# Kernel optimization log

Measured on AMD Instinct MI355X. Metric: run time of the kernel, lower is better.

The kernel has to match this reference:

```python
import jax, jax.numpy as jnp
import numpy as np

B, C, CI, H, W = 8, 256, 128, 48, 48


def conv1x1(x, w, b):
    # x: (B,C,H,W), w: (CI,C), b: (CI,)
    return jnp.einsum('bchw,oc->bohw', x, w) + b[None, :, None, None]


def setup_inputs() -> dict:
    key = jax.random.key(0)
    ks = jax.random.split(key, 14)
    s = 1.0 / np.sqrt(C)
    d = {
        'x_1': jax.random.normal(ks[0], (B, C, H, W), jnp.float32),
        'x_2': jax.random.normal(ks[1], (B, C, H, W), jnp.float32),
    }
    names = ['v1', 'k1', 'q1', 'v2', 'k2', 'q2']
    for i, n in enumerate(names):
        d['w_' + n] = jax.random.uniform(ks[2 + 2 * i], (CI, C), jnp.float32, -s, s)
        d['b_' + n] = jax.random.uniform(ks[3 + 2 * i], (CI,), jnp.float32, -s, s)
    return d


def reference(x_1, x_2, w_v1, b_v1, w_k1, b_k1, w_q1, b_q1,
              w_v2, b_v2, w_k2, b_k2, w_q2, b_q2):
    b, ci, h, w = x_1.shape[0], w_v1.shape[0], x_1.shape[2], x_1.shape[3]
    n = h * w
    V1 = conv1x1(x_1, w_v1, b_v1).reshape(b, ci, n)
    K1 = conv1x1(x_1, w_k1, b_k1).reshape(b, ci, n)
    Q1 = conv1x1(x_1, w_q1, b_q1).reshape(b, ci, n)
    V2 = conv1x1(x_2, w_v2, b_v2).reshape(b, ci, n)
    K2 = conv1x1(x_2, w_k2, b_k2).reshape(b, ci, n)
    Q2 = conv1x1(x_2, w_q2, b_q2).reshape(b, ci, n)
    # sigmoid-gated cross attention, (B, N, N)
    R12 = jax.nn.sigmoid(jnp.einsum('bcn,bcm->bnm', Q1, K2))
    R21 = jax.nn.sigmoid(jnp.einsum('bcn,bcm->bnm', Q2, K1))
    Fu1 = jnp.einsum('bnm,bcm->bcn', R12, V2).reshape(b, ci, h, w)
    Fu2 = jnp.einsum('bnm,bcm->bcn', R21, V1).reshape(b, ci, h, w)
    y_1 = jnp.concatenate([x_1, Fu1], axis=1)
    y_2 = jnp.concatenate([x_2, Fu2], axis=1)
    return (y_1, y_2)
```

## Files before the change

### kernel.cpp

```cpp
#include <hip/hip_runtime.h>
#include <hip/hip_bf16.h>


typedef __bf16 bf16;
typedef __bf16 bf16x8 __attribute__((ext_vector_type(8)));
typedef __bf16 bf16x4 __attribute__((ext_vector_type(4)));
typedef float f32x4 __attribute__((ext_vector_type(4)));
typedef float f32x16 __attribute__((ext_vector_type(16)));
typedef unsigned int u32x4 __attribute__((ext_vector_type(4)));

#define NB 8
#define NC 256
#define NCI 128
#define NHW 2304
#define NT32 72

__global__ __launch_bounds__(256) void wconv_kernel(
    const float* __restrict__ w0, const float* __restrict__ w1,
    const float* __restrict__ w2, const float* __restrict__ w3,
    const float* __restrict__ w4, const float* __restrict__ w5,
    bf16* __restrict__ dst)
{
    int idx = (blockIdx.x * 256 + threadIdx.x) * 8;
    int m = idx >> 15;
    int off = idx & 32767;
    const float* w = (m == 0) ? w0 : (m == 1) ? w1 : (m == 2) ? w2
                   : (m == 3) ? w3 : (m == 4) ? w4 : w5;
    f32x4 a0 = *(const f32x4*)(w + off);
    f32x4 a1 = *(const f32x4*)(w + off + 4);
    bf16x8 o;
    #pragma unroll
    for (int j = 0; j < 4; ++j) { o[j] = (bf16)a0[j]; o[4 + j] = (bf16)a1[j]; }
    *(bf16x8*)(dst + idx) = o;
}

__global__ __launch_bounds__(256) void qkv_kernel(
    const float* __restrict__ x1, const float* __restrict__ x2,
    const bf16* __restrict__ wb,
    const float* __restrict__ bv1, const float* __restrict__ bk1, const float* __restrict__ bq1,
    const float* __restrict__ bv2, const float* __restrict__ bk2, const float* __restrict__ bq2,
    bf16* __restrict__ Qt, bf16* __restrict__ Kt, bf16* __restrict__ Vt,
    float* __restrict__ out)
{
    __shared__ __align__(16) bf16 Xt[32 * 264];

    int gid = blockIdx.x;
    int nt = gid % NT32;
    int s = (gid / NT32) & 1;
    int b = gid / (2 * NT32);
    int n0 = nt * 32;

    const float* x = s ? x2 : x1;
    const bf16* wv = wb + (size_t)(s * 3 + 0) * (NCI * NC);
    const bf16* wk = wb + (size_t)(s * 3 + 1) * (NCI * NC);
    const bf16* wq = wb + (size_t)(s * 3 + 2) * (NCI * NC);
    const float* bv = s ? bv2 : bv1;
    const float* bk = s ? bk2 : bk1;
    const float* bq = s ? bq2 : bq1;
    float* outy = out + (size_t)s * (NB * 384 * NHW);

    int tid = threadIdx.x;
    {
        int n_off = (tid & 3) * 8;
        int c0l = tid >> 2;
        #pragma unroll
        for (int i = 0; i < 4; ++i) {
            int c = c0l + i * 64;
            const float* src = x + ((size_t)(b * NC + c) * NHW + n0 + n_off);
            f32x4 a0 = *(const f32x4*)src;
            f32x4 a1 = *(const f32x4*)(src + 4);
            float* dsty = outy + ((size_t)(b * 384 + c) * NHW + n0 + n_off);
            *(f32x4*)dsty = a0;
            *(f32x4*)(dsty + 4) = a1;
            #pragma unroll
            for (int j = 0; j < 4; ++j) {
                Xt[(n_off + j) * 264 + c] = (bf16)a0[j];
                Xt[(n_off + 4 + j) * 264 + c] = (bf16)a1[j];
            }
        }
    }
    __syncthreads();

    int lane = tid & 63;
    int wid = tid >> 6;
    int row = lane & 15, quad = lane >> 4;
    int ci_base = wid * 32;

    f32x4 acc[3][2][2];
    #pragma unroll
    for (int t = 0; t < 3; ++t)
        #pragma unroll
        for (int mi = 0; mi < 2; ++mi)
            #pragma unroll
            for (int j = 0; j < 2; ++j)
                acc[t][mi][j] = (f32x4){0.f, 0.f, 0.f, 0.f};

    const bf16* wptr[3] = {wq, wk, wv};
    #pragma unroll
    for (int ks = 0; ks < 8; ++ks) {
        int c0 = ks * 32 + quad * 8;
        bf16x8 bfrag[2];
        #pragma unroll
        for (int j = 0; j < 2; ++j)
            bfrag[j] = *(const bf16x8*)&Xt[(j * 16 + row) * 264 + c0];
        #pragma unroll
        for (int t = 0; t < 3; ++t) {
            #pragma unroll
            for (int mi = 0; mi < 2; ++mi) {
                bf16x8 afrag = *(const bf16x8*)&wptr[t][(size_t)(ci_base + mi * 16 + row) * NC + c0];
                #pragma unroll
                for (int j = 0; j < 2; ++j)
                    acc[t][mi][j] = __builtin_amdgcn_mfma_f32_16x16x32_bf16(
                        afrag, bfrag[j], acc[t][mi][j], 0, 0, 0);
            }
        }
    }

    size_t qkbase = ((size_t)s * NB + b) * NHW * NCI;
    size_t vbase  = ((size_t)s * NB + b) * NCI * NHW;
    #pragma unroll
    for (int mi = 0; mi < 2; ++mi) {
        int ci0 = ci_base + mi * 16 + quad * 4;
        f32x4 bq4 = *(const f32x4*)&bq[ci0];
        f32x4 bk4 = *(const f32x4*)&bk[ci0];
        f32x4 bv4 = *(const f32x4*)&bv[ci0];
        #pragma unroll
        for (int j = 0; j < 2; ++j) {
            int n = n0 + j * 16 + row;
            bf16x4 pk;
            #pragma unroll
            for (int r = 0; r < 4; ++r) pk[r] = (bf16)(acc[0][mi][j][r] + bq4[r]);
            *(bf16x4*)&Qt[qkbase + (size_t)n * NCI + ci0] = pk;
            #pragma unroll
            for (int r = 0; r < 4; ++r) pk[r] = (bf16)(acc[1][mi][j][r] + bk4[r]);
            *(bf16x4*)&Kt[qkbase + (size_t)n * NCI + ci0] = pk;
            #pragma unroll
            for (int r = 0; r < 4; ++r)
                Vt[vbase + (size_t)(ci0 + r) * NHW + n] = (bf16)(acc[2][mi][j][r] + bv4[r]);
        }
    }
}

__global__ __launch_bounds__(512, 2) void attn_kernel(
    const bf16* __restrict__ Qt, const bf16* __restrict__ Kt, const bf16* __restrict__ Vt,
    float* __restrict__ out)
{
    __shared__ __align__(16) bf16 SMEM[40960];
    bf16* KQ = SMEM;
    bf16* VQ = SMEM + 16384;
    bf16* QL = SMEM + 32768;

    int gid = blockIdx.x;
    int pair = (gid & 7) * 2 + ((gid >> 3) & 1);
    int nb = gid >> 4;
    int dir = pair & 1;
    int b = pair >> 1;

    int tid = threadIdx.x;
    int lane = tid & 63;
    int w = tid >> 6;
    int ns = w & 1;
    int mq = w >> 1;
    int col = lane & 31;
    int hi = lane >> 5;

    int sq = dir, skv = dir ^ 1;
    const bf16* q = Qt + ((size_t)sq  * NB + b) * (NHW * NCI);
    const bf16* k = Kt + ((size_t)skv * NB + b) * (NHW * NCI);
    const bf16* v = Vt + ((size_t)skv * NB + b) * (NCI * NHW);
    float* outy = out + (size_t)dir * (NB * 384 * NHW) + ((size_t)b * 384 + 256) * NHW;

    #pragma unroll
    for (int i = 0; i < 2; ++i) {
        int c = tid + i * 512;
        int qr = c >> 4, qc = c & 15;
        bf16x8 t = *(const bf16x8*)&q[(size_t)(nb * 64 + qr) * NCI + qc * 8];
        *(bf16x8*)&QL[qr * 128 + ((qc ^ (qr & 15)) * 8)] = t;
    }

    int kgoff[4], vgoff[4], kloff[4], vloff[4];
    #pragma unroll
    for (int i = 0; i < 4; ++i) {
        int c = tid + i * 512;
        int qd = c >> 9, cc = c & 511;
        int kr = cc >> 4, kc = cc & 15;
        kgoff[i] = (qd * 576 + kr) * NCI + kc * 8;
        kloff[i] = qd * 4096 + kr * 128 + ((kc ^ (kr & 15)) * 8);
        int vr = cc >> 2, vc = cc & 3;
        vgoff[i] = vr * NHW + qd * 576 + vc * 8;
        vloff[i] = qd * 4096 + vr * 32 + ((vc ^ ((vr >> 1) & 3)) * 8);
    }

    int nw = nb * 64 + ns * 32;

    f32x16 o0, o1, o2, o3;
    #pragma unroll
    for (int j = 0; j < 16; ++j) { o0[j] = 0.f; o1[j] = 0.f; o2[j] = 0.f; o3[j] = 0.f; }

    bf16x8 rk[4], rv[4];
    #pragma unroll
    for (int i = 0; i < 4; ++i) {
        rk[i] = *(const bf16x8*)(k + kgoff[i]);
        rv[i] = *(const bf16x8*)(v + vgoff[i]);
    }

    int krd = mq * 4096 + col * 128;
    int qrd = (ns * 32 + col) * 128;
    int cswz = col & 15;
    int vsw = (col >> 1) & 3;
    int vrd = mq * 4096 + col * 32;

    for (int it = 0; it < 18; ++it) {
        __syncthreads();
        #pragma unroll
        for (int i = 0; i < 4; ++i) {
            *(bf16x8*)&KQ[kloff[i]] = rk[i];
            *(bf16x8*)&VQ[vloff[i]] = rv[i];
        }
        __syncthreads();

        f32x16 s;
        #pragma unroll
        for (int j = 0; j < 16; ++j) s[j] = 0.f;

        __builtin_amdgcn_s_setprio(1);
        #pragma unroll
        for (int kq = 0; kq < 8; ++kq) {
            int ch = ((2 * kq + hi) ^ cswz) * 8;
            bf16x8 kf = *(const bf16x8*)&KQ[krd + ch];
            bf16x8 qf = *(const bf16x8*)&QL[qrd + ch];
            s = __builtin_amdgcn_mfma_f32_32x32x16_bf16(kf, qf, s, 0, 0, 0);
        }
        __builtin_amdgcn_s_setprio(0);

        float p[16];
        #pragma unroll
        for (int r = 0; r < 16; ++r) {
            float e = __expf(-s[r]);
            p[r] = __builtin_amdgcn_rcpf(1.0f + e);
        }
        u32x4 pbw[2];
        #pragma unroll
        for (int kst = 0; kst < 2; ++kst) {
            unsigned int a0, a1, b0, b1;
            asm("v_cvt_pk_bf16_f32 %0, %1, %2" : "=v"(a0) : "v"(p[8*kst+0]), "v"(p[8*kst+1]));
            asm("v_cvt_pk_bf16_f32 %0, %1, %2" : "=v"(a1) : "v"(p[8*kst+2]), "v"(p[8*kst+3]));
            asm("v_cvt_pk_bf16_f32 %0, %1, %2" : "=v"(b0) : "v"(p[8*kst+4]), "v"(p[8*kst+5]));
            asm("v_cvt_pk_bf16_f32 %0, %1, %2" : "=v"(b1) : "v"(p[8*kst+6]), "v"(p[8*kst+7]));
            asm volatile("v_permlane32_swap_b32 %0, %1" : "+v"(a0), "+v"(b0));
            asm volatile("v_permlane32_swap_b32 %0, %1" : "+v"(a1), "+v"(b1));
            pbw[kst] = (u32x4){a0, a1, b0, b1};
        }

        if (it < 17) {
            size_t ko = (size_t)(it + 1) * 4096;
            int vo = (it + 1) * 32;
            #pragma unroll
            for (int i = 0; i < 4; ++i) {
                rk[i] = *(const bf16x8*)(k + ko + kgoff[i]);
                rv[i] = *(const bf16x8*)(v + vo + vgoff[i]);
            }
        }

        __builtin_amdgcn_s_setprio(1);
        #pragma unroll
        for (int km = 0; km < 2; ++km) {
            bf16x8 pf = __builtin_bit_cast(bf16x8, pbw[km]);
            int mch = ((2 * km + hi) ^ vsw) * 8;
            {
                bf16x8 vf = *(const bf16x8*)&VQ[vrd + 0 * 1024 + mch];
                o0 = __builtin_amdgcn_mfma_f32_32x32x16_bf16(vf, pf, o0, 0, 0, 0);
            }
            {
                bf16x8 vf = *(const bf16x8*)&VQ[vrd + 1 * 1024 + mch];
                o1 = __builtin_amdgcn_mfma_f32_32x32x16_bf16(vf, pf, o1, 0, 0, 0);
            }
            {
                bf16x8 vf = *(const bf16x8*)&VQ[vrd + 2 * 1024 + mch];
                o2 = __builtin_amdgcn_mfma_f32_32x32x16_bf16(vf, pf, o2, 0, 0, 0);
            }
            {
                bf16x8 vf = *(const bf16x8*)&VQ[vrd + 3 * 1024 + mch];
                o3 = __builtin_amdgcn_mfma_f32_32x32x16_bf16(vf, pf, o3, 0, 0, 0);
            }
        }
        __builtin_amdgcn_s_setprio(0);
    }

    float* RED = (float*)SMEM;

    auto wpart = [&](float* buf, const f32x16& a, int cb) {
        #pragma unroll
        for (int g = 0; g < 4; ++g) {
            f32x4 v4;
            #pragma unroll
            for (int j = 0; j < 4; ++j) v4[j] = a[g * 4 + j];
            *(f32x4*)&buf[lane * 64 + (((cb * 4 + g) ^ (lane & 15)) * 4)] = v4;
        }
    };
    auto rpart = [&](float* buf, f32x16& a, int cb) {
        #pragma unroll
        for (int g = 0; g < 4; ++g) {
            f32x4 v4 = *(const f32x4*)&buf[lane * 64 + (((cb * 4 + g) ^ (lane & 15)) * 4)];
            #pragma unroll
            for (int j = 0; j < 4; ++j) a[g * 4 + j] += v4[j];
        }
    };

    __syncthreads();
    if (mq >= 2) {
        float* buf = RED + (ns * 2 + (mq & 1)) * 4096;
        wpart(buf, o0, 0); wpart(buf, o1, 1); wpart(buf, o2, 2); wpart(buf, o3, 3);
    }
    __syncthreads();
    if (mq < 2) {
        float* buf = RED + (ns * 2 + mq) * 4096;
        rpart(buf, o0, 0); rpart(buf, o1, 1); rpart(buf, o2, 2); rpart(buf, o3, 3);
    }
    __syncthreads();
    if (mq == 1) {
        float* buf = RED + ns * 4096;
        wpart(buf, o0, 0); wpart(buf, o1, 1); wpart(buf, o2, 2); wpart(buf, o3, 3);
    }
    __syncthreads();
    if (mq == 0) {
        float* buf = RED + ns * 4096;
        rpart(buf, o0, 0); rpart(buf, o1, 1); rpart(buf, o2, 2); rpart(buf, o3, 3);
        #pragma unroll
        for (int r = 0; r < 16; ++r) {
            int cr = (r & 3) + 8 * (r >> 2) + 4 * hi;
            outy[(size_t)(0 * 32 + cr) * NHW + nw + col] = o0[r];
            outy[(size_t)(1 * 32 + cr) * NHW + nw + col] = o1[r];
            outy[(size_t)(2 * 32 + cr) * NHW + nw + col] = o2[r];
            outy[(size_t)(3 * 32 + cr) * NHW + nw + col] = o3[r];
        }
    }
}

extern "C" void kernel_launch(void* const* d_in, const int* in_sizes, int n_in,
                              void* d_out, int out_size, void* d_ws, size_t ws_size,
                              hipStream_t stream) {
    const float* x1  = (const float*)d_in[0];
    const float* x2  = (const float*)d_in[1];
    const float* wv1 = (const float*)d_in[2];  const float* bv1 = (const float*)d_in[3];
    const float* wk1 = (const float*)d_in[4];  const float* bk1 = (const float*)d_in[5];
    const float* wq1 = (const float*)d_in[6];  const float* bq1 = (const float*)d_in[7];
    const float* wv2 = (const float*)d_in[8];  const float* bv2 = (const float*)d_in[9];
    const float* wk2 = (const float*)d_in[10]; const float* bk2 = (const float*)d_in[11];
    const float* wq2 = (const float*)d_in[12]; const float* bq2 = (const float*)d_in[13];
    float* out = (float*)d_out;

    size_t per = (size_t)2 * NB * NHW * NCI;
    bf16* Qt = (bf16*)d_ws;
    bf16* Kt = Qt + per;
    bf16* Vt = Kt + per;
    bf16* wb = Vt + per;

    wconv_kernel<<<dim3(96), dim3(256), 0, stream>>>(wv1, wk1, wq1, wv2, wk2, wq2, wb);

    qkv_kernel<<<dim3(NB * 2 * NT32), dim3(256), 0, stream>>>(
        x1, x2, wb, bv1, bk1, bq1, bv2, bk2, bq2, Qt, Kt, Vt, out);

    attn_kernel<<<dim3(NB * 2 * 36), dim3(512), 0, stream>>>(Qt, Kt, Vt, out);
}
```

Before: 244.1 us.

## Restructure attention block to 4 waves with Q fragments held in registers

```diff
diff --git a/kernel.cpp b/kernel.cpp
--- a/kernel.cpp
+++ b/kernel.cpp
@@ -141,18 +141,17 @@
     }
 }
 
-__global__ __launch_bounds__(512, 2) void attn_kernel(
+__global__ __launch_bounds__(256, 3) void attn_kernel(
     const bf16* __restrict__ Qt, const bf16* __restrict__ Kt, const bf16* __restrict__ Vt,
     float* __restrict__ out)
 {
-    __shared__ __align__(16) bf16 SMEM[40960];
-    bf16* KQ = SMEM;
-    bf16* VQ = SMEM + 16384;
-    bf16* QL = SMEM + 32768;
+    __shared__ __align__(16) bf16 SMEM[16384];
+    bf16* KH = SMEM;
+    bf16* VH = SMEM + 8192;
 
     int gid = blockIdx.x;
     int pair = (gid & 7) * 2 + ((gid >> 3) & 1);
-    int nb = gid >> 4;
+    int nt = gid >> 4;
     int dir = pair & 1;
     int b = pair >> 1;
 
@@ -160,7 +159,7 @@
     int lane = tid & 63;
     int w = tid >> 6;
     int ns = w & 1;
-    int mq = w >> 1;
+    int mh = w >> 1;
     int col = lane & 31;
     int hi = lane >> 5;
 
@@ -170,28 +169,25 @@
     const bf16* v = Vt + ((size_t)skv * NB + b) * (NCI * NHW);
     float* outy = out + (size_t)dir * (NB * 384 * NHW) + ((size_t)b * 384 + 256) * NHW;
 
-    #pragma unroll
-    for (int i = 0; i < 2; ++i) {
-        int c = tid + i * 512;
-        int qr = c >> 4, qc = c & 15;
-        bf16x8 t = *(const bf16x8*)&q[(size_t)(nb * 64 + qr) * NCI + qc * 8];
-        *(bf16x8*)&QL[qr * 128 + ((qc ^ (qr & 15)) * 8)] = t;
-    }
-
     int kgoff[4], vgoff[4], kloff[4], vloff[4];
     #pragma unroll
     for (int i = 0; i < 4; ++i) {
-        int c = tid + i * 512;
-        int qd = c >> 9, cc = c & 511;
+        int c = tid + i * 256;
+        int hs = c >> 9;
+        int cc = c & 511;
         int kr = cc >> 4, kc = cc & 15;
-        kgoff[i] = (qd * 576 + kr) * NCI + kc * 8;
-        kloff[i] = qd * 4096 + kr * 128 + ((kc ^ (kr & 15)) * 8);
+        kgoff[i] = (hs * 1152 + kr) * NCI + kc * 8;
+        kloff[i] = hs * 4096 + kr * 128 + ((kc ^ (kr & 15)) * 8);
         int vr = cc >> 2, vc = cc & 3;
-        vgoff[i] = vr * NHW + qd * 576 + vc * 8;
-        vloff[i] = qd * 4096 + vr * 32 + ((vc ^ ((vr >> 1) & 3)) * 8);
-    }
-
-    int nw = nb * 64 + ns * 32;
+        vgoff[i] = vr * NHW + hs * 1152 + vc * 8;
+        vloff[i] = hs * 4096 + vr * 32 + ((vc ^ ((vr >> 1) & 3)) * 8);
+    }
+
+    int nw = nt * 64 + ns * 32;
+    bf16x8 qf[8];
+    #pragma unroll
+    for (int kq = 0; kq < 8; ++kq)
+        qf[kq] = *(const bf16x8*)&q[(size_t)(nw + col) * NCI + kq * 16 + hi * 8];
 
     f32x16 o0, o1, o2, o3;
     #pragma unroll
@@ -204,20 +200,28 @@
         rv[i] = *(const bf16x8*)(v + vgoff[i]);
     }
 
-    int krd = mq * 4096 + col * 128;
-    int qrd = (ns * 32 + col) * 128;
+    const bf16* KB = &KH[mh * 4096];
+    const bf16* VB = &VH[mh * 4096];
     int cswz = col & 15;
     int vsw = (col >> 1) & 3;
-    int vrd = mq * 4096 + col * 32;
-
-    for (int it = 0; it < 18; ++it) {
+
+    for (int it = 0; it < 36; ++it) {
         __syncthreads();
         #pragma unroll
         for (int i = 0; i < 4; ++i) {
-            *(bf16x8*)&KQ[kloff[i]] = rk[i];
-            *(bf16x8*)&VQ[vloff[i]] = rv[i];
+            *(bf16x8*)&KH[kloff[i]] = rk[i];
+            *(bf16x8*)&VH[vloff[i]] = rv[i];
         }
         __syncthreads();
+        if (it < 35) {
+            size_t ko = (size_t)(it + 1) * 32 * NCI;
+            int vo = (it + 1) * 32;
+            #pragma unroll
+            for (int i = 0; i < 4; ++i) {
+                rk[i] = *(const bf16x8*)(k + ko + kgoff[i]);
+                rv[i] = *(const bf16x8*)(v + vo + vgoff[i]);
+            }
+        }
 
         f32x16 s;
         #pragma unroll
@@ -226,10 +230,8 @@
         __builtin_amdgcn_s_setprio(1);
         #pragma unroll
         for (int kq = 0; kq < 8; ++kq) {
-            int ch = ((2 * kq + hi) ^ cswz) * 8;
-            bf16x8 kf = *(const bf16x8*)&KQ[krd + ch];
-            bf16x8 qf = *(const bf16x8*)&QL[qrd + ch];
-            s = __builtin_amdgcn_mfma_f32_32x32x16_bf16(kf, qf, s, 0, 0, 0);
+            bf16x8 kf = *(const bf16x8*)&KB[col * 128 + (((2 * kq + hi) ^ cswz) * 8)];
+            s = __builtin_amdgcn_mfma_f32_32x32x16_bf16(kf, qf[kq], s, 0, 0, 0);
         }
         __builtin_amdgcn_s_setprio(0);
 
@@ -252,35 +254,25 @@
             pbw[kst] = (u32x4){a0, a1, b0, b1};
         }
 
-        if (it < 17) {
-            size_t ko = (size_t)(it + 1) * 4096;
-            int vo = (it + 1) * 32;
-            #pragma unroll
-            for (int i = 0; i < 4; ++i) {
-                rk[i] = *(const bf16x8*)(k + ko + kgoff[i]);
-                rv[i] = *(const bf16x8*)(v + vo + vgoff[i]);
-            }
-        }
-
         __builtin_amdgcn_s_setprio(1);
         #pragma unroll
         for (int km = 0; km < 2; ++km) {
             bf16x8 pf = __builtin_bit_cast(bf16x8, pbw[km]);
             int mch = ((2 * km + hi) ^ vsw) * 8;
             {
-                bf16x8 vf = *(const bf16x8*)&VQ[vrd + 0 * 1024 + mch];
+                bf16x8 vf = *(const bf16x8*)&VB[(0 * 32 + col) * 32 + mch];
                 o0 = __builtin_amdgcn_mfma_f32_32x32x16_bf16(vf, pf, o0, 0, 0, 0);
             }
             {
-                bf16x8 vf = *(const bf16x8*)&VQ[vrd + 1 * 1024 + mch];
+                bf16x8 vf = *(const bf16x8*)&VB[(1 * 32 + col) * 32 + mch];
                 o1 = __builtin_amdgcn_mfma_f32_32x32x16_bf16(vf, pf, o1, 0, 0, 0);
             }
             {
-                bf16x8 vf = *(const bf16x8*)&VQ[vrd + 2 * 1024 + mch];
+                bf16x8 vf = *(const bf16x8*)&VB[(2 * 32 + col) * 32 + mch];
                 o2 = __builtin_amdgcn_mfma_f32_32x32x16_bf16(vf, pf, o2, 0, 0, 0);
             }
             {
-                bf16x8 vf = *(const bf16x8*)&VQ[vrd + 3 * 1024 + mch];
+                bf16x8 vf = *(const bf16x8*)&VB[(3 * 32 + col) * 32 + mch];
                 o3 = __builtin_amdgcn_mfma_f32_32x32x16_bf16(vf, pf, o3, 0, 0, 0);
             }
         }
@@ -288,43 +280,30 @@
     }
 
     float* RED = (float*)SMEM;
-
-    auto wpart = [&](float* buf, const f32x16& a, int cb) {
+    float* buf = RED + ns * 4096;
+
+    auto wpart = [&](float* bp, const f32x16& a, int cb) {
         #pragma unroll
         for (int g = 0; g < 4; ++g) {
             f32x4 v4;
             #pragma unroll
             for (int j = 0; j < 4; ++j) v4[j] = a[g * 4 + j];
-            *(f32x4*)&buf[lane * 64 + (((cb * 4 + g) ^ (lane & 15)) * 4)] = v4;
+            *(f32x4*)&bp[lane * 64 + (((cb * 4 + g) ^ (lane & 15)) * 4)] = v4;
         }
     };
-    auto rpart = [&](float* buf, f32x16& a, int cb) {
+    auto rpart = [&](float* bp, f32x16& a, int cb) {
         #pragma unroll
         for (int g = 0; g < 4; ++g) {
-            f32x4 v4 = *(const f32x4*)&buf[lane * 64 + (((cb * 4 + g) ^ (lane & 15)) * 4)];
+            f32x4 v4 = *(const f32x4*)&bp[lane * 64 + (((cb * 4 + g) ^ (lane & 15)) * 4)];
             #pragma unroll
             for (int j = 0; j < 4; ++j) a[g * 4 + j] += v4[j];
         }
     };
 
     __syncthreads();
-    if (mq >= 2) {
-        float* buf = RED + (ns * 2 + (mq & 1)) * 4096;
-        wpart(buf, o0, 0); wpart(buf, o1, 1); wpart(buf, o2, 2); wpart(buf, o3, 3);
-    }
+    if (mh == 1) { wpart(buf, o0, 0); wpart(buf, o1, 1); wpart(buf, o2, 2); wpart(buf, o3, 3); }
     __syncthreads();
-    if (mq < 2) {
-        float* buf = RED + (ns * 2 + mq) * 4096;
-        rpart(buf, o0, 0); rpart(buf, o1, 1); rpart(buf, o2, 2); rpart(buf, o3, 3);
-    }
-    __syncthreads();
-    if (mq == 1) {
-        float* buf = RED + ns * 4096;
-        wpart(buf, o0, 0); wpart(buf, o1, 1); wpart(buf, o2, 2); wpart(buf, o3, 3);
-    }
-    __syncthreads();
-    if (mq == 0) {
-        float* buf = RED + ns * 4096;
+    if (mh == 0) {
         rpart(buf, o0, 0); rpart(buf, o1, 1); rpart(buf, o2, 2); rpart(buf, o3, 3);
         #pragma unroll
         for (int r = 0; r < 16; ++r) {
@@ -361,5 +340,5 @@
     qkv_kernel<<<dim3(NB * 2 * NT32), dim3(256), 0, stream>>>(
         x1, x2, wb, bv1, bk1, bq1, bv2, bk2, bq2, Qt, Kt, Vt, out);
 
-    attn_kernel<<<dim3(NB * 2 * 36), dim3(512), 0, stream>>>(Qt, Kt, Vt, out);
+    attn_kernel<<<dim3(NB * 2 * 36), dim3(256), 0, stream>>>(Qt, Kt, Vt, out);
 }
```

After: 263.6 us. +8.0%, slower.
